# Kernel optimization log

Hardware: AMD Instinct MI355X
Metric: run time of the kernel (lower is better)

## Reference

```python
import jax, jax.numpy as jnp
import numpy as np

NUM_HEADS = 8
SPARSITY = 0.25
BOUNDARY_W = 0.5
LN_EPS = 1e-5


def setup_inputs() -> dict:
    key = jax.random.key(0)
    ks = jax.random.split(key, 16)
    B, C, H, W = 8, 256, 64, 64
    Ch = C // 4
    s = lambda *sh: 1.0 / np.sqrt(sh[-1])
    inp = {
        'x': jax.random.normal(ks[0], (B, C, H, W), jnp.float32),
        'boundary_map': jax.random.uniform(ks[1], (B, 1, H, W), jnp.float32),
        'imp_w1': jax.random.normal(ks[2], (Ch, C), jnp.float32) * s(C),
        'imp_b1': jnp.zeros((Ch,), jnp.float32),
        'imp_w2': jax.random.normal(ks[3], (1, Ch), jnp.float32) * s(Ch),
        'imp_b2': jnp.zeros((1,), jnp.float32),
        'wq': jax.random.normal(ks[4], (C, C), jnp.float32) * s(C),
        'bq': jnp.zeros((C,), jnp.float32),
        'wk': jax.random.normal(ks[5], (C, C), jnp.float32) * s(C),
        'bk': jnp.zeros((C,), jnp.float32),
        'wv': jax.random.normal(ks[6], (C, C), jnp.float32) * s(C),
        'bv': jnp.zeros((C,), jnp.float32),
        'wo': jax.random.normal(ks[7], (C, C), jnp.float32) * (0.1 * s(C)),
        'bo': jnp.zeros((C,), jnp.float32),
        'ln_g': jnp.ones((C,), jnp.float32),
        'ln_b': jnp.zeros((C,), jnp.float32),
    }
    return inp


def reference(x, boundary_map, imp_w1, imp_b1, imp_w2, imp_b2,
              wq, bq, wk, bk, wv, bv, wo, bo, ln_g, ln_b):
    B, C, H, W = x.shape
    N = H * W
    K = max(int(N * SPARSITY), 1)
    nh = NUM_HEADS
    hd = C // nh
    scale = hd ** -0.5

    # importance net: 1x1 conv -> GELU -> 1x1 conv -> sigmoid
    h = jnp.einsum('bchw,oc->bohw', x, imp_w1) + imp_b1[None, :, None, None]
    h = jax.nn.gelu(h, approximate=False)
    imp = jnp.einsum('bchw,oc->bohw', h, imp_w2) + imp_b2[None, :, None, None]
    importance = jax.nn.sigmoid(imp) + BOUNDARY_W * boundary_map  # [B,1,H,W]

    # top-K token selection
    _, top_idx = jax.lax.top_k(importance.reshape(B, N), K)  # [B,K]

    x_flat = x.transpose(0, 2, 3, 1).reshape(B, N, C)
    x_sp = jnp.take_along_axis(x_flat, top_idx[..., None], axis=1)  # [B,K,C]

    # sparse self-attention over K tokens
    q = (jnp.einsum('bkc,oc->bko', x_sp, wq) + bq).reshape(B, K, nh, hd)
    k = (jnp.einsum('bkc,oc->bko', x_sp, wk) + bk).reshape(B, K, nh, hd)
    v = (jnp.einsum('bkc,oc->bko', x_sp, wv) + bv).reshape(B, K, nh, hd)
    attn = jax.nn.softmax(jnp.einsum('bqhd,bkhd->bhqk', q, k) * scale, axis=-1)
    o = jnp.einsum('bhqk,bkhd->bqhd', attn, v).reshape(B, K, C)
    out_sp = jnp.einsum('bkc,oc->bko', o, wo) + bo

    # residual + LayerNorm
    y = out_sp + x_sp
    mu = jnp.mean(y, axis=-1, keepdims=True)
    var = jnp.mean(jnp.square(y - mu), axis=-1, keepdims=True)
    enh = (y - mu) * jax.lax.rsqrt(var + LN_EPS) * ln_g + ln_b  # [B,K,C]

    # scatter enhanced tokens back
    bidx = jnp.arange(B)[:, None]
    out_full = x_flat.at[bidx, top_idx].set(enh)
    out = out_full.reshape(B, H, W, C).transpose(0, 3, 1, 2)
    return out, importance
```

## Files before the change

kernel.cpp:

```cpp
#include <hip/hip_runtime.h>
#include <math.h>

#define B_ 8
#define C_ 256
#define N_ 4096
#define K_ 1024
#define NH_ 8
#define HD_ 32

typedef __attribute__((ext_vector_type(8))) short short8;
typedef __attribute__((ext_vector_type(8))) _Float16 half8;
typedef __attribute__((ext_vector_type(4))) _Float16 half4;
typedef __attribute__((ext_vector_type(4))) float f32x4;

#if __has_builtin(__builtin_amdgcn_exp2f)
#define EXPX(x) __builtin_amdgcn_exp2f(x)
#define QSCALE (0.17677669529663688f * 1.4426950408889634f)
#else
#define EXPX(x) __expf(x)
#define QSCALE 0.17677669529663688f
#endif

__device__ __forceinline__ unsigned bfr(float x){
  unsigned u = __float_as_uint(x);
  return (u + 0x7FFFu + ((u >> 16) & 1u)) >> 16;
}
__device__ __forceinline__ unsigned pk2(float lo, float hi){
  return bfr(lo) | (bfr(hi) << 16);
}
__device__ __forceinline__ unsigned hpk(float a, float b){
  _Float16 ha = (_Float16)a, hb = (_Float16)b;
  unsigned short ua = __builtin_bit_cast(unsigned short, ha);
  unsigned short ub = __builtin_bit_cast(unsigned short, hb);
  return (unsigned)ua | ((unsigned)ub << 16);
}
__device__ __forceinline__ half4 pk4rtz(float a, float b, float c, float d){
  auto lo = __builtin_amdgcn_cvt_pkrtz(a, b);
  auto hi = __builtin_amdgcn_cvt_pkrtz(c, d);
  uint2 u = make_uint2(__builtin_bit_cast(unsigned, lo), __builtin_bit_cast(unsigned, hi));
  return __builtin_bit_cast(half4, u);
}

__global__ __launch_bounds__(256) void w2h_kernel(
    const float* __restrict__ wq, const float* __restrict__ wk,
    const float* __restrict__ wv, const float* __restrict__ wo,
    unsigned short* __restrict__ wh)
{
  const float* src = blockIdx.y==0 ? wq : blockIdx.y==1 ? wk : blockIdx.y==2 ? wv : wo;
  const int e = (blockIdx.x*256 + threadIdx.x)*8;
  float4 a = *(const float4*)(src + e);
  float4 b = *(const float4*)(src + e + 4);
  uint4 o;
  o.x = hpk(a.x, a.y); o.y = hpk(a.z, a.w);
  o.z = hpk(b.x, b.y); o.w = hpk(b.z, b.w);
  *(uint4*)(wh + (size_t)blockIdx.y*65536 + e) = o;
}

__global__ __launch_bounds__(256) void imp_kernel(
    const float* __restrict__ x, const float* __restrict__ bmap,
    const float* __restrict__ w1, const float* __restrict__ b1,
    const float* __restrict__ w2, const float* __restrict__ b2,
    float* __restrict__ imp_out)
{
  __shared__ float xs[64][256];
  const int t = threadIdx.x;
  const int b = blockIdx.x >> 6, tile = blockIdx.x & 63;
  const int n0 = tile * 64;
  {
    const int i = t & 63, cg = t >> 6;
    const float* xb = x + (size_t)b*C_*N_ + n0 + i;
    const int ib = (i & 15) ^ (i >> 2);
    #pragma unroll 4
    for (int cc = 0; cc < 16; cc++){
      const int c0 = cg*64 + cc*4;
      float4 v;
      v.x = xb[(size_t)(c0+0)*N_];
      v.y = xb[(size_t)(c0+1)*N_];
      v.z = xb[(size_t)(c0+2)*N_];
      v.w = xb[(size_t)(c0+3)*N_];
      *(float4*)&xs[i][4*((cg*16+cc) ^ ib)] = v;
    }
  }
  __syncthreads();
  const int pg = t & 15, og = t >> 4;
  float acc[4][4];
  #pragma unroll
  for (int pp=0;pp<4;pp++)
    #pragma unroll
    for (int oo=0;oo<4;oo++) acc[pp][oo] = 0.f;
  int pb[4];
  #pragma unroll
  for (int pp=0;pp<4;pp++){ int p = 4*pg+pp; pb[pp] = (p&15)^(p>>2); }
  #pragma unroll 2
  for (int c8 = 0; c8 < 256; c8 += 8){
    const int G = c8 >> 2;
    float4 xa[4], xc[4];
    #pragma unroll
    for (int pp=0;pp<4;pp++){
      xa[pp] = *(const float4*)&xs[4*pg+pp][4*( G    ^ pb[pp])];
      xc[pp] = *(const float4*)&xs[4*pg+pp][4*((G+1) ^ pb[pp])];
    }
    float4 wa[4], wb[4];
    #pragma unroll
    for (int oo=0;oo<4;oo++){
      const float* wr = w1 + (size_t)(4*og+oo)*C_ + c8;
      wa[oo] = *(const float4*)wr;
      wb[oo] = *(const float4*)(wr+4);
    }
    #pragma unroll
    for (int pp=0;pp<4;pp++)
      #pragma unroll
      for (int oo=0;oo<4;oo++)
        acc[pp][oo] += xa[pp].x*wa[oo].x + xa[pp].y*wa[oo].y + xa[pp].z*wa[oo].z + xa[pp].w*wa[oo].w
                     + xc[pp].x*wb[oo].x + xc[pp].y*wb[oo].y + xc[pp].z*wb[oo].z + xc[pp].w*wb[oo].w;
  }
  float part[4] = {0.f,0.f,0.f,0.f};
  #pragma unroll
  for (int oo=0;oo<4;oo++){
    const int o = 4*og + oo;
    const float b1o = b1[o], w2o = w2[o];
    #pragma unroll
    for (int pp=0;pp<4;pp++){
      float a = acc[pp][oo] + b1o;
      float g = 0.5f*a*(1.f + erff(a*0.70710678118654752f));
      part[pp] += w2o*g;
    }
  }
  #pragma unroll
  for (int pp=0;pp<4;pp++){
    part[pp] += __shfl_xor(part[pp], 16);
    part[pp] += __shfl_xor(part[pp], 32);
  }
  __syncthreads();
  float* red = &xs[0][0];
  const int w = t >> 6;
  if ((t & 63) < 16){
    #pragma unroll
    for (int pp=0;pp<4;pp++) red[w*64 + 4*(t&15)+pp] = part[pp];
  }
  __syncthreads();
  if (t < 64){
    float s = red[t]+red[64+t]+red[128+t]+red[192+t] + b2[0];
    float sig = 1.f/(1.f+expf(-s));
    imp_out[(size_t)b*N_ + n0 + t] = sig + 0.5f*bmap[(size_t)b*N_ + n0 + t];
  }
}

__global__ __launch_bounds__(1024) void topk_kernel(const float* __restrict__ imp, int* __restrict__ tidx)
{
  __shared__ unsigned long long s[4096];
  __shared__ int idx[1024];
  const int b = blockIdx.x, t = threadIdx.x;
  const float* ib = imp + (size_t)b*N_;
  for (int m = t; m < N_; m += 1024){
    unsigned u = __float_as_uint(ib[m]);
    u = (u & 0x80000000u) ? ~u : (u | 0x80000000u);
    s[m] = ((unsigned long long)u << 32) | (unsigned)(~m);
  }
  for (int k = 2; k <= 4096; k <<= 1){
    for (int j = k >> 1; j > 0; j >>= 1){
      __syncthreads();
      #pragma unroll 2
      for (int m = t; m < 2048; m += 1024){
        int i = 2*m - (m & (j-1));
        int l = i + j;
        unsigned long long a = s[i], c = s[l];
        if ((a > c) == ((i & k) == 0)){ s[i] = c; s[l] = a; }
      }
    }
  }
  __syncthreads();
  idx[t] = (int)(~(unsigned)(s[3072 + t]));
  for (int k = 2; k <= 1024; k <<= 1){
    for (int j = k >> 1; j > 0; j >>= 1){
      __syncthreads();
      if (t < 512){
        int i = 2*t - (t & (j-1));
        int l = i + j;
        int a = idx[i], c = idx[l];
        if ((a > c) == ((i & k) == 0)){ idx[i] = c; idx[l] = a; }
      }
    }
  }
  __syncthreads();
  tidx[(size_t)b*K_ + t] = idx[t];
}

__global__ __launch_bounds__(512) void qkv_kernel(
    const float* __restrict__ x, const int* __restrict__ tidx,
    const unsigned short* __restrict__ wh,
    const float* __restrict__ bq, const float* __restrict__ bk, const float* __restrict__ bv,
    float* __restrict__ xsp, unsigned short* __restrict__ qbf,
    unsigned short* __restrict__ kbf, unsigned short* __restrict__ vtb)
{
  __shared__ unsigned short xsb[16][256];
  const int t = threadIdx.x;
  const int kt = blockIdx.x, b = blockIdx.y;
  const int tok0 = kt*16;
  {
    const int i = t & 15, jg = t >> 4;
    const int n = tidx[(size_t)b*K_ + tok0 + i];
    const float* xb = x + (size_t)b*C_*N_ + n;
    float v[8];
    #pragma unroll
    for (int u = 0; u < 8; u++) v[u] = xb[(size_t)(jg*8+u)*N_];
    float* xr = xsp + ((size_t)b*K_ + tok0 + i)*C_ + jg*8;
    *(float4*)(xr)     = make_float4(v[0],v[1],v[2],v[3]);
    *(float4*)(xr + 4) = make_float4(v[4],v[5],v[6],v[7]);
    uint4 pw;
    pw.x = hpk(v[0],v[1]); pw.y = hpk(v[2],v[3]);
    pw.z = hpk(v[4],v[5]); pw.w = hpk(v[6],v[7]);
    *(uint4*)((char*)&xsb[0][0] + i*512 + ((jg ^ (i&7))*16)) = pw;
  }
  __syncthreads();

  const int lane = t & 63, w = t >> 6;
  const int g = lane >> 4, c = lane & 15;

  f32x4 acc[3][2];
  #pragma unroll
  for (int s=0;s<3;s++)
    #pragma unroll
    for (int j=0;j<2;j++) acc[s][j] = (f32x4){0.f,0.f,0.f,0.f};

  #pragma unroll 1
  for (int ks = 0; ks < 8; ks++){
    half8 Xf = *(const half8*)((const char*)&xsb[0][0] + c*512 + (((4*ks+g) ^ (c&7))*16));
    half8 Wf[3][2];
    #pragma unroll
    for (int s=0;s<3;s++)
      #pragma unroll
      for (int j=0;j<2;j++)
        Wf[s][j] = *(const half8*)(wh + (size_t)s*65536 + (32*w + 16*j + c)*C_ + ks*32 + 8*g);
    acc[0][0] = __builtin_amdgcn_mfma_f32_16x16x32_f16(Wf[0][0], Xf, acc[0][0], 0,0,0);
    acc[0][1] = __builtin_amdgcn_mfma_f32_16x16x32_f16(Wf[0][1], Xf, acc[0][1], 0,0,0);
    acc[1][0] = __builtin_amdgcn_mfma_f32_16x16x32_f16(Wf[1][0], Xf, acc[1][0], 0,0,0);
    acc[1][1] = __builtin_amdgcn_mfma_f32_16x16x32_f16(Wf[1][1], Xf, acc[1][1], 0,0,0);
    acc[2][0] = __builtin_amdgcn_mfma_f32_16x16x32_f16(Xf, Wf[2][0], acc[2][0], 0,0,0);
    acc[2][1] = __builtin_amdgcn_mfma_f32_16x16x32_f16(Xf, Wf[2][1], acc[2][1], 0,0,0);
  }

  const int bh = b*NH_ + w;
  #pragma unroll
  for (int s=0;s<2;s++){
    const float* bias = s ? bk : bq;
    const float sc = s ? 1.f : QSCALE;
    unsigned short* dstb = s ? kbf : qbf;
    #pragma unroll
    for (int j=0;j<2;j++){
      f32x4 a = acc[s][j];
      float4 bb = *(const float4*)(bias + w*32 + 16*j + 4*g);
      unsigned lo = pk2((a[0]+bb.x)*sc, (a[1]+bb.y)*sc);
      unsigned hi = pk2((a[2]+bb.z)*sc, (a[3]+bb.w)*sc);
      unsigned short* dst = dstb + ((size_t)bh*K_ + tok0 + c)*HD_ + 16*j + 4*g;
      *(uint2*)dst = make_uint2(lo, hi);
    }
  }
  const int base32 = tok0 & ~31;
  const int half   = (tok0 >> 4) & 1;
  #pragma unroll
  for (int j=0;j<2;j++){
    f32x4 a = acc[2][j];
    const float bvv = bv[w*32 + 16*j + c];
    unsigned lo = hpk(a[0]+bvv, a[1]+bvv);
    unsigned hi = hpk(a[2]+bvv, a[3]+bvv);
    unsigned short* dst = vtb + ((size_t)bh*HD_ + 16*j + c)*K_ + base32 + 8*g + 4*half;
    *(uint2*)dst = make_uint2(lo, hi);
  }
}

__global__ __launch_bounds__(512) void attn_kernel(
    const unsigned short* __restrict__ qbf, const unsigned short* __restrict__ kbf,
    const unsigned short* __restrict__ vtb, unsigned short* __restrict__ ob)
{
  __shared__ float po[4][64][19];
  const int tid = threadIdx.x;
  const int t = tid & 63, w = tid >> 6;
  const int sp = w >> 2, qq = w & 3;
  const int flat = blockIdx.x;
  const int h = flat & 7;
  const int rest = flat >> 3;
  const int qt = rest & 7;
  const int b = rest >> 3;
  const int g = t >> 4, c = t & 15;
  const int bh = b*NH_ + h;
  const int q0 = qt*128 + qq*32;

  short8 Qf0 = *(const short8*)(qbf + ((size_t)bh*K_ + q0 + c)*HD_ + g*8);
  short8 Qf1 = *(const short8*)(qbf + ((size_t)bh*K_ + q0 + 16 + c)*HD_ + g*8);

  const int kbeg = sp*512;
  const unsigned short* kp  = kbf + (size_t)bh*K_*HD_ + (size_t)(kbeg + c)*HD_ + g*8;
  const unsigned short* vp0 = vtb + ((size_t)bh*HD_ + c)*K_ + kbeg + g*8;
  const unsigned short* vp1 = vp0 + (size_t)16*K_;

  const half4 ONES = {(_Float16)1.f, (_Float16)1.f, (_Float16)1.f, (_Float16)1.f};
  f32x4 ot00 = {0.f,0.f,0.f,0.f}, ot01 = {0.f,0.f,0.f,0.f};
  f32x4 ot10 = {0.f,0.f,0.f,0.f}, ot11 = {0.f,0.f,0.f,0.f};
  f32x4 otL0 = {0.f,0.f,0.f,0.f}, otL1 = {0.f,0.f,0.f,0.f};

  short8 K0c = *(const short8*)(kp);
  short8 K1c = *(const short8*)(kp + 16*HD_);
  half8  V0c = *(const half8*)(vp0);
  half8  V1c = *(const half8*)(vp1);

  #pragma unroll 2
  for (int it = 0; it < 16; ++it){
    kp += 32*HD_; vp0 += 32; vp1 += 32;
    short8 K0n = *(const short8*)(kp);
    short8 K1n = *(const short8*)(kp + 16*HD_);
    half8  V0n = *(const half8*)(vp0);
    half8  V1n = *(const half8*)(vp1);

    f32x4 z = {0.f,0.f,0.f,0.f};
    __builtin_amdgcn_s_setprio(1);
    f32x4 s00 = __builtin_amdgcn_mfma_f32_16x16x32_bf16(K0c, Qf0, z, 0, 0, 0);
    f32x4 s01 = __builtin_amdgcn_mfma_f32_16x16x32_bf16(K1c, Qf0, z, 0, 0, 0);
    f32x4 s10 = __builtin_amdgcn_mfma_f32_16x16x32_bf16(K0c, Qf1, z, 0, 0, 0);
    f32x4 s11 = __builtin_amdgcn_mfma_f32_16x16x32_bf16(K1c, Qf1, z, 0, 0, 0);
    __builtin_amdgcn_s_setprio(0);

    float p00[4], p01[4], p10[4], p11[4];
    #pragma unroll
    for (int r=0;r<4;r++){
      p00[r] = EXPX(s00[r]); p01[r] = EXPX(s01[r]);
      p10[r] = EXPX(s10[r]); p11[r] = EXPX(s11[r]);
    }

    half4 P00 = pk4rtz(p00[0], p00[1], p00[2], p00[3]);
    half4 P01 = pk4rtz(p01[0], p01[1], p01[2], p01[3]);
    half4 P10 = pk4rtz(p10[0], p10[1], p10[2], p10[3]);
    half4 P11 = pk4rtz(p11[0], p11[1], p11[2], p11[3]);

    half4 A0lo = __builtin_shufflevector(V0c, V0c, 0, 1, 2, 3);
    half4 A0hi = __builtin_shufflevector(V0c, V0c, 4, 5, 6, 7);
    half4 A1lo = __builtin_shufflevector(V1c, V1c, 0, 1, 2, 3);
    half4 A1hi = __builtin_shufflevector(V1c, V1c, 4, 5, 6, 7);

    __builtin_amdgcn_s_setprio(1);
    ot00 = __builtin_amdgcn_mfma_f32_16x16x16f16(A0lo, P00, ot00, 0, 0, 0);
    ot00 = __builtin_amdgcn_mfma_f32_16x16x16f16(A0hi, P01, ot00, 0, 0, 0);
    ot01 = __builtin_amdgcn_mfma_f32_16x16x16f16(A1lo, P00, ot01, 0, 0, 0);
    ot01 = __builtin_amdgcn_mfma_f32_16x16x16f16(A1hi, P01, ot01, 0, 0, 0);
    ot10 = __builtin_amdgcn_mfma_f32_16x16x16f16(A0lo, P10, ot10, 0, 0, 0);
    ot10 = __builtin_amdgcn_mfma_f32_16x16x16f16(A0hi, P11, ot10, 0, 0, 0);
    ot11 = __builtin_amdgcn_mfma_f32_16x16x16f16(A1lo, P10, ot11, 0, 0, 0);
    ot11 = __builtin_amdgcn_mfma_f32_16x16x16f16(A1hi, P11, ot11, 0, 0, 0);
    otL0 = __builtin_amdgcn_mfma_f32_16x16x16f16(ONES, P00, otL0, 0, 0, 0);
    otL0 = __builtin_amdgcn_mfma_f32_16x16x16f16(ONES, P01, otL0, 0, 0, 0);
    otL1 = __builtin_amdgcn_mfma_f32_16x16x16f16(ONES, P10, otL1, 0, 0, 0);
    otL1 = __builtin_amdgcn_mfma_f32_16x16x16f16(ONES, P11, otL1, 0, 0, 0);
    __builtin_amdgcn_s_setprio(0);

    K0c = K0n; K1c = K1n; V0c = V0n; V1c = V1n;
  }

  if (sp == 1){
    float* d = po[qq][t];
    d[0]=ot00[0]; d[1]=ot00[1]; d[2]=ot00[2];  d[3]=ot00[3];
    d[4]=ot01[0]; d[5]=ot01[1]; d[6]=ot01[2];  d[7]=ot01[3];
    d[8]=ot10[0]; d[9]=ot10[1]; d[10]=ot10[2]; d[11]=ot10[3];
    d[12]=ot11[0];d[13]=ot11[1];d[14]=ot11[2]; d[15]=ot11[3];
    d[16]=otL0[0]; d[17]=otL1[0];
  }
  __syncthreads();
  if (sp == 0){
    const float* d = po[qq][t];
    ot00[0]+=d[0]; ot00[1]+=d[1]; ot00[2]+=d[2];  ot00[3]+=d[3];
    ot01[0]+=d[4]; ot01[1]+=d[5]; ot01[2]+=d[6];  ot01[3]+=d[7];
    ot10[0]+=d[8]; ot10[1]+=d[9]; ot10[2]+=d[10]; ot10[3]+=d[11];
    ot11[0]+=d[12];ot11[1]+=d[13];ot11[2]+=d[14]; ot11[3]+=d[15];
    const float L0 = otL0[0] + d[16];
    const float L1 = otL1[0] + d[17];
    const float i0 = 1.f / L0, i1 = 1.f / L1;
    unsigned short* o0 = ob + ((size_t)b*K_ + q0 + c)*C_ + h*HD_;
    unsigned short* o1 = ob + ((size_t)b*K_ + q0 + 16 + c)*C_ + h*HD_;
    *(uint2*)(o0 + 4*g)      = make_uint2(hpk(ot00[0]*i0, ot00[1]*i0), hpk(ot00[2]*i0, ot00[3]*i0));
    *(uint2*)(o0 + 16 + 4*g) = make_uint2(hpk(ot01[0]*i0, ot01[1]*i0), hpk(ot01[2]*i0, ot01[3]*i0));
    *(uint2*)(o1 + 4*g)      = make_uint2(hpk(ot10[0]*i1, ot10[1]*i1), hpk(ot10[2]*i1, ot10[3]*i1));
    *(uint2*)(o1 + 16 + 4*g) = make_uint2(hpk(ot11[0]*i1, ot11[1]*i1), hpk(ot11[2]*i1, ot11[3]*i1));
  }
}

__global__ __launch_bounds__(512) void out_kernel(
    const unsigned short* __restrict__ ob, const float* __restrict__ xsp,
    const int* __restrict__ tidx, const unsigned short* __restrict__ woh, const float* __restrict__ bo,
    const float* __restrict__ lng, const float* __restrict__ lnb,
    float* __restrict__ out)
{
  __shared__ float red1[8][64], red2[8][64];
  __shared__ float mus[64], rss[64];
  __shared__ int nn[64];
  const int t = threadIdx.x;
  const int kt = blockIdx.x, b = blockIdx.y;
  const int tok0 = kt*64;
  const int lane = t & 63, w = t >> 6;
  const int g = lane >> 4, c = lane & 15;

  if (t < 64) nn[t] = tidx[(size_t)b*K_ + tok0 + t];

  f32x4 acc[2][4];
  #pragma unroll
  for (int j=0;j<2;j++)
    #pragma unroll
    for (int tt=0;tt<4;tt++) acc[j][tt] = (f32x4){0.f,0.f,0.f,0.f};

  const unsigned short* ob0 = ob + ((size_t)b*K_ + tok0)*C_;
  const unsigned short* wr0 = woh + (32*w + c)*C_;

  #pragma unroll 1
  for (int ks = 0; ks < 8; ks++){
    half8 Wf0 = *(const half8*)(wr0 + ks*32 + 8*g);
    half8 Wf1 = *(const half8*)(wr0 + 16*C_ + ks*32 + 8*g);
    #pragma unroll
    for (int tt=0;tt<4;tt++){
      half8 Of = *(const half8*)(ob0 + (size_t)(16*tt + c)*C_ + ks*32 + 8*g);
      acc[0][tt] = __builtin_amdgcn_mfma_f32_16x16x32_f16(Wf0, Of, acc[0][tt], 0,0,0);
      acc[1][tt] = __builtin_amdgcn_mfma_f32_16x16x32_f16(Wf1, Of, acc[1][tt], 0,0,0);
    }
  }

  float4 bb[2];
  #pragma unroll
  for (int j=0;j<2;j++) bb[j] = *(const float4*)(bo + 32*w + 16*j + 4*g);
  #pragma unroll
  for (int tt=0;tt<4;tt++){
    const float* xr = xsp + ((size_t)b*K_ + tok0 + 16*tt + c)*C_ + 32*w + 4*g;
    #pragma unroll
    for (int j=0;j<2;j++){
      float4 xv = *(const float4*)(xr + 16*j);
      acc[j][tt][0] += bb[j].x + xv.x;
      acc[j][tt][1] += bb[j].y + xv.y;
      acc[j][tt][2] += bb[j].z + xv.z;
      acc[j][tt][3] += bb[j].w + xv.w;
    }
  }

  #pragma unroll
  for (int tt=0;tt<4;tt++){
    float s1 = 0.f, s2 = 0.f;
    #pragma unroll
    for (int j=0;j<2;j++)
      #pragma unroll
      for (int r=0;r<4;r++){ float y = acc[j][tt][r]; s1 += y; s2 += y*y; }
    s1 += __shfl_xor(s1, 16); s2 += __shfl_xor(s2, 16);
    s1 += __shfl_xor(s1, 32); s2 += __shfl_xor(s2, 32);
    if (g == 0){ red1[w][16*tt + c] = s1; red2[w][16*tt + c] = s2; }
  }
  __syncthreads();
  if (t < 64){
    float a = 0.f, q2 = 0.f;
    #pragma unroll
    for (int ww=0;ww<8;ww++){ a += red1[ww][t]; q2 += red2[ww][t]; }
    float mu = a*(1.f/256.f);
    float var = q2*(1.f/256.f) - mu*mu;
    mus[t] = mu;
    rss[t] = rsqrtf(var + 1e-5f);
  }
  __syncthreads();

  float4 gv[2], bv2[2];
  #pragma unroll
  for (int j=0;j<2;j++){
    gv[j]  = *(const float4*)(lng + 32*w + 16*j + 4*g);
    bv2[j] = *(const float4*)(lnb + 32*w + 16*j + 4*g);
  }
  float* outb = out + (size_t)b*C_*N_;
  #pragma unroll
  for (int tt=0;tt<4;tt++){
    const int tok = 16*tt + c;
    const float mu = mus[tok], rs = rss[tok];
    const int n = nn[tok];
    #pragma unroll
    for (int j=0;j<2;j++){
      const int oc0 = 32*w + 16*j + 4*g;
      const float* gvp = (const float*)&gv[j];
      const float* bvp = (const float*)&bv2[j];
      #pragma unroll
      for (int r=0;r<4;r++)
        outb[(size_t)(oc0 + r)*N_ + n] = (acc[j][tt][r]-mu)*rs*gvp[r] + bvp[r];
    }
  }
}

extern "C" void kernel_launch(void* const* d_in, const int* in_sizes, int n_in,
                              void* d_out, int out_size, void* d_ws, size_t ws_size,
                              hipStream_t stream)
{
  const float* x    = (const float*)d_in[0];
  const float* bmap = (const float*)d_in[1];
  const float* w1   = (const float*)d_in[2];
  const float* b1   = (const float*)d_in[3];
  const float* w2   = (const float*)d_in[4];
  const float* b2   = (const float*)d_in[5];
  const float* wq   = (const float*)d_in[6];
  const float* bq   = (const float*)d_in[7];
  const float* wk   = (const float*)d_in[8];
  const float* bk   = (const float*)d_in[9];
  const float* wv   = (const float*)d_in[10];
  const float* bv   = (const float*)d_in[11];
  const float* wo   = (const float*)d_in[12];
  const float* bo   = (const float*)d_in[13];
  const float* lng  = (const float*)d_in[14];
  const float* lnb  = (const float*)d_in[15];

  float* out = (float*)d_out;
  float* imp_out = out + (size_t)B_*C_*N_;

  char* wsb = (char*)d_ws;
  int*   tidx = (int*)wsb;
  float* xsp  = (float*)(wsb + 65536);
  unsigned short* ob16 = (unsigned short*)(xsp + (size_t)B_*K_*C_);
  unsigned short* qbf = ob16 + 2*(size_t)B_*K_*C_;
  unsigned short* kbf = qbf + (size_t)B_*NH_*K_*HD_;
  unsigned short* vtb = kbf + (size_t)B_*NH_*K_*HD_;
  unsigned short* wh  = vtb + (size_t)B_*NH_*K_*HD_;

  hipMemcpyAsync(out, x, (size_t)B_*C_*N_*sizeof(float), hipMemcpyDeviceToDevice, stream);
  w2h_kernel <<<dim3(32, 4),    dim3(256),  0, stream>>>(wq, wk, wv, wo, wh);
  imp_kernel <<<dim3(512),      dim3(256),  0, stream>>>(x, bmap, w1, b1, w2, b2, imp_out);
  topk_kernel<<<dim3(8),        dim3(1024), 0, stream>>>(imp_out, tidx);
  qkv_kernel <<<dim3(64, 8),    dim3(512),  0, stream>>>(x, tidx, wh, bq, bk, bv, xsp, qbf, kbf, vtb);
  attn_kernel<<<dim3(512),      dim3(512),  0, stream>>>(qbf, kbf, vtb, ob16);
  out_kernel <<<dim3(16, 8),    dim3(512),  0, stream>>>(ob16, xsp, tidx, wh + 3*65536, bo, lng, lnb, out);
}
```

Before: 159.6 us.

## Fuse residual copy into importance kernel and replace top-k index sort with compaction

The separate device-to-device copy of x into the output is folded into the importance kernel, which now writes x to the output while staging it, and runs with 512 threads. The second bitonic sort over selected indices in top-k becomes a threshold test plus prefix-sum compaction, which keeps indices in ascending order without another sort. The attention loop is unrolled by hand with two-stage register prefetch, and the output kernel processes 32 tokens per block so more blocks are launched. Together these target extra memory traffic, sort synchronisation and latency hiding, at the cost of more register pressure and threshold logic that depends on unique keys.

```diff
diff --git a/kernel.cpp b/kernel.cpp
--- a/kernel.cpp
+++ b/kernel.cpp
@@ -56,11 +56,11 @@
   *(uint4*)(wh + (size_t)blockIdx.y*65536 + e) = o;
 }
 
-__global__ __launch_bounds__(256) void imp_kernel(
+__global__ __launch_bounds__(512) void imp_kernel(
     const float* __restrict__ x, const float* __restrict__ bmap,
     const float* __restrict__ w1, const float* __restrict__ b1,
     const float* __restrict__ w2, const float* __restrict__ b2,
-    float* __restrict__ imp_out)
+    float* __restrict__ imp_out, float* __restrict__ outx)
 {
   __shared__ float xs[64][256];
   const int t = threadIdx.x;
@@ -69,25 +69,30 @@
   {
     const int i = t & 63, cg = t >> 6;
     const float* xb = x + (size_t)b*C_*N_ + n0 + i;
-    const int ib = (i & 15) ^ (i >> 2);
-    #pragma unroll 4
-    for (int cc = 0; cc < 16; cc++){
-      const int c0 = cg*64 + cc*4;
+    float* ox = outx + (size_t)b*C_*N_ + n0 + i;
+    const int ib2 = (i & 15) ^ (i >> 2);
+    #pragma unroll
+    for (int cc = 0; cc < 8; cc++){
+      const int c0 = cg*32 + cc*4;
       float4 v;
       v.x = xb[(size_t)(c0+0)*N_];
       v.y = xb[(size_t)(c0+1)*N_];
       v.z = xb[(size_t)(c0+2)*N_];
       v.w = xb[(size_t)(c0+3)*N_];
-      *(float4*)&xs[i][4*((cg*16+cc) ^ ib)] = v;
-    }
-  }
-  __syncthreads();
-  const int pg = t & 15, og = t >> 4;
-  float acc[4][4];
+      *(float4*)&xs[i][4*((cg*8+cc) ^ ib2)] = v;
+      ox[(size_t)(c0+0)*N_] = v.x;
+      ox[(size_t)(c0+1)*N_] = v.y;
+      ox[(size_t)(c0+2)*N_] = v.z;
+      ox[(size_t)(c0+3)*N_] = v.w;
+    }
+  }
+  __syncthreads();
+  const int pg = t & 15, og2 = t >> 4;
+  float acc[4][2];
   #pragma unroll
   for (int pp=0;pp<4;pp++)
     #pragma unroll
-    for (int oo=0;oo<4;oo++) acc[pp][oo] = 0.f;
+    for (int oo=0;oo<2;oo++) acc[pp][oo] = 0.f;
   int pb[4];
   #pragma unroll
   for (int pp=0;pp<4;pp++){ int p = 4*pg+pp; pb[pp] = (p&15)^(p>>2); }
@@ -100,24 +105,24 @@
       xa[pp] = *(const float4*)&xs[4*pg+pp][4*( G    ^ pb[pp])];
       xc[pp] = *(const float4*)&xs[4*pg+pp][4*((G+1) ^ pb[pp])];
     }
-    float4 wa[4], wb[4];
-    #pragma unroll
-    for (int oo=0;oo<4;oo++){
-      const float* wr = w1 + (size_t)(4*og+oo)*C_ + c8;
+    float4 wa[2], wb[2];
+    #pragma unroll
+    for (int oo=0;oo<2;oo++){
+      const float* wr = w1 + (size_t)(2*og2+oo)*C_ + c8;
       wa[oo] = *(const float4*)wr;
       wb[oo] = *(const float4*)(wr+4);
     }
     #pragma unroll
     for (int pp=0;pp<4;pp++)
       #pragma unroll
-      for (int oo=0;oo<4;oo++)
+      for (int oo=0;oo<2;oo++)
         acc[pp][oo] += xa[pp].x*wa[oo].x + xa[pp].y*wa[oo].y + xa[pp].z*wa[oo].z + xa[pp].w*wa[oo].w
                      + xc[pp].x*wb[oo].x + xc[pp].y*wb[oo].y + xc[pp].z*wb[oo].z + xc[pp].w*wb[oo].w;
   }
   float part[4] = {0.f,0.f,0.f,0.f};
   #pragma unroll
-  for (int oo=0;oo<4;oo++){
-    const int o = 4*og + oo;
+  for (int oo=0;oo<2;oo++){
+    const int o = 2*og2 + oo;
     const float b1o = b1[o], w2o = w2[o];
     #pragma unroll
     for (int pp=0;pp<4;pp++){
@@ -133,14 +138,17 @@
   }
   __syncthreads();
   float* red = &xs[0][0];
-  const int w = t >> 6;
-  if ((t & 63) < 16){
-    #pragma unroll
-    for (int pp=0;pp<4;pp++) red[w*64 + 4*(t&15)+pp] = part[pp];
+  const int w = t >> 6, lane = t & 63;
+  if (lane < 16){
+    #pragma unroll
+    for (int pp=0;pp<4;pp++) red[w*64 + 4*lane + pp] = part[pp];
   }
   __syncthreads();
   if (t < 64){
-    float s = red[t]+red[64+t]+red[128+t]+red[192+t] + b2[0];
+    float s = 0.f;
+    #pragma unroll
+    for (int ww=0;ww<8;ww++) s += red[ww*64 + t];
+    s += b2[0];
     float sig = 1.f/(1.f+expf(-s));
     imp_out[(size_t)b*N_ + n0 + t] = sig + 0.5f*bmap[(size_t)b*N_ + n0 + t];
   }
@@ -149,7 +157,7 @@
 __global__ __launch_bounds__(1024) void topk_kernel(const float* __restrict__ imp, int* __restrict__ tidx)
 {
   __shared__ unsigned long long s[4096];
-  __shared__ int idx[1024];
+  __shared__ int ws2[16];
   const int b = blockIdx.x, t = threadIdx.x;
   const float* ib = imp + (size_t)b*N_;
   for (int m = t; m < N_; m += 1024){
@@ -170,20 +178,34 @@
     }
   }
   __syncthreads();
-  idx[t] = (int)(~(unsigned)(s[3072 + t]));
-  for (int k = 2; k <= 1024; k <<= 1){
-    for (int j = k >> 1; j > 0; j >>= 1){
-      __syncthreads();
-      if (t < 512){
-        int i = 2*t - (t & (j-1));
-        int l = i + j;
-        int a = idx[i], c = idx[l];
-        if ((a > c) == ((i & k) == 0)){ idx[i] = c; idx[l] = a; }
-      }
-    }
-  }
-  __syncthreads();
-  tidx[(size_t)b*K_ + t] = idx[t];
+  const unsigned long long thr = s[3072];
+  int sel[4]; int cnt = 0;
+  #pragma unroll
+  for (int u2 = 0; u2 < 4; u2++){
+    const int m = 4*t + u2;
+    unsigned u = __float_as_uint(ib[m]);
+    u = (u & 0x80000000u) ? ~u : (u | 0x80000000u);
+    unsigned long long key = ((unsigned long long)u << 32) | (unsigned)(~m);
+    sel[u2] = (key >= thr) ? 1 : 0;
+    cnt += sel[u2];
+  }
+  int incl = cnt;
+  #pragma unroll
+  for (int d2 = 1; d2 < 64; d2 <<= 1){
+    int v2 = __shfl_up(incl, d2);
+    if ((t & 63) >= d2) incl += v2;
+  }
+  if ((t & 63) == 63) ws2[t >> 6] = incl;
+  __syncthreads();
+  int base = 0;
+  const int wv2 = t >> 6;
+  #pragma unroll
+  for (int ww = 0; ww < 16; ww++) if (ww < wv2) base += ws2[ww];
+  int pos = base + incl - cnt;
+  #pragma unroll
+  for (int u2 = 0; u2 < 4; u2++){
+    if (sel[u2]) tidx[(size_t)b*K_ + pos++] = 4*t + u2;
+  }
 }
 
 __global__ __launch_bounds__(512) void qkv_kernel(
@@ -299,61 +321,71 @@
   f32x4 ot10 = {0.f,0.f,0.f,0.f}, ot11 = {0.f,0.f,0.f,0.f};
   f32x4 otL0 = {0.f,0.f,0.f,0.f}, otL1 = {0.f,0.f,0.f,0.f};
 
-  short8 K0c = *(const short8*)(kp);
-  short8 K1c = *(const short8*)(kp + 16*HD_);
-  half8  V0c = *(const half8*)(vp0);
-  half8  V1c = *(const half8*)(vp1);
-
-  #pragma unroll 2
-  for (int it = 0; it < 16; ++it){
+#define ATTN_STEP(K0c,K1c,V0c,V1c) do {                                           \
+    f32x4 z = {0.f,0.f,0.f,0.f};                                                  \
+    __builtin_amdgcn_s_setprio(1);                                                \
+    f32x4 s00 = __builtin_amdgcn_mfma_f32_16x16x32_bf16(K0c, Qf0, z, 0, 0, 0);    \
+    f32x4 s01 = __builtin_amdgcn_mfma_f32_16x16x32_bf16(K1c, Qf0, z, 0, 0, 0);    \
+    f32x4 s10 = __builtin_amdgcn_mfma_f32_16x16x32_bf16(K0c, Qf1, z, 0, 0, 0);    \
+    f32x4 s11 = __builtin_amdgcn_mfma_f32_16x16x32_bf16(K1c, Qf1, z, 0, 0, 0);    \
+    __builtin_amdgcn_s_setprio(0);                                                \
+    float p00[4], p01[4], p10[4], p11[4];                                         \
+    _Pragma("unroll")                                                             \
+    for (int r=0;r<4;r++){                                                        \
+      p00[r] = EXPX(s00[r]); p01[r] = EXPX(s01[r]);                               \
+      p10[r] = EXPX(s10[r]); p11[r] = EXPX(s11[r]);                               \
+    }                                                                             \
+    half4 P00 = pk4rtz(p00[0], p00[1], p00[2], p00[3]);                           \
+    half4 P01 = pk4rtz(p01[0], p01[1], p01[2], p01[3]);                           \
+    half4 P10 = pk4rtz(p10[0], p10[1], p10[2], p10[3]);                           \
+    half4 P11 = pk4rtz(p11[0], p11[1], p11[2], p11[3]);                           \
+    half4 A0lo = __builtin_shufflevector(V0c, V0c, 0, 1, 2, 3);                   \
+    half4 A0hi = __builtin_shufflevector(V0c, V0c, 4, 5, 6, 7);                   \
+    half4 A1lo = __builtin_shufflevector(V1c, V1c, 0, 1, 2, 3);                   \
+    half4 A1hi = __builtin_shufflevector(V1c, V1c, 4, 5, 6, 7);                   \
+    __builtin_amdgcn_s_setprio(1);                                                \
+    ot00 = __builtin_amdgcn_mfma_f32_16x16x16f16(A0lo, P00, ot00, 0, 0, 0);       \
+    ot00 = __builtin_amdgcn_mfma_f32_16x16x16f16(A0hi, P01, ot00, 0, 0, 0);       \
+    ot01 = __builtin_amdgcn_mfma_f32_16x16x16f16(A1lo, P00, ot01, 0, 0, 0);       \
+    ot01 = __builtin_amdgcn_mfma_f32_16x16x16f16(A1hi, P01, ot01, 0, 0, 0);       \
+    ot10 = __builtin_amdgcn_mfma_f32_16x16x16f16(A0lo, P10, ot10, 0, 0, 0);       \
+    ot10 = __builtin_amdgcn_mfma_f32_16x16x16f16(A0hi, P11, ot10, 0, 0, 0);       \
+    ot11 = __builtin_amdgcn_mfma_f32_16x16x16f16(A1lo, P10, ot11, 0, 0, 0);       \
+    ot11 = __builtin_amdgcn_mfma_f32_16x16x16f16(A1hi, P11, ot11, 0, 0, 0);       \
+    otL0 = __builtin_amdgcn_mfma_f32_16x16x16f16(ONES, P00, otL0, 0, 0, 0);       \
+    otL0 = __builtin_amdgcn_mfma_f32_16x16x16f16(ONES, P01, otL0, 0, 0, 0);       \
+    otL1 = __builtin_amdgcn_mfma_f32_16x16x16f16(ONES, P10, otL1, 0, 0, 0);       \
+    otL1 = __builtin_amdgcn_mfma_f32_16x16x16f16(ONES, P11, otL1, 0, 0, 0);       \
+    __builtin_amdgcn_s_setprio(0);                                                \
+  } while(0)
+
+  short8 K0a = *(const short8*)(kp);
+  short8 K1a = *(const short8*)(kp + 16*HD_);
+  half8  V0a = *(const half8*)(vp0);
+  half8  V1a = *(const half8*)(vp1);
+  kp += 32*HD_; vp0 += 32; vp1 += 32;
+  short8 K0b = *(const short8*)(kp);
+  short8 K1b = *(const short8*)(kp + 16*HD_);
+  half8  V0b = *(const half8*)(vp0);
+  half8  V1b = *(const half8*)(vp1);
+
+  for (int it = 0; it < 16; it += 2){
     kp += 32*HD_; vp0 += 32; vp1 += 32;
     short8 K0n = *(const short8*)(kp);
     short8 K1n = *(const short8*)(kp + 16*HD_);
     half8  V0n = *(const half8*)(vp0);
     half8  V1n = *(const half8*)(vp1);
-
-    f32x4 z = {0.f,0.f,0.f,0.f};
-    __builtin_amdgcn_s_setprio(1);
-    f32x4 s00 = __builtin_amdgcn_mfma_f32_16x16x32_bf16(K0c, Qf0, z, 0, 0, 0);
-    f32x4 s01 = __builtin_amdgcn_mfma_f32_16x16x32_bf16(K1c, Qf0, z, 0, 0, 0);
-    f32x4 s10 = __builtin_amdgcn_mfma_f32_16x16x32_bf16(K0c, Qf1, z, 0, 0, 0);
-    f32x4 s11 = __builtin_amdgcn_mfma_f32_16x16x32_bf16(K1c, Qf1, z, 0, 0, 0);
-    __builtin_amdgcn_s_setprio(0);
-
-    float p00[4], p01[4], p10[4], p11[4];
-    #pragma unroll
-    for (int r=0;r<4;r++){
-      p00[r] = EXPX(s00[r]); p01[r] = EXPX(s01[r]);
-      p10[r] = EXPX(s10[r]); p11[r] = EXPX(s11[r]);
-    }
-
-    half4 P00 = pk4rtz(p00[0], p00[1], p00[2], p00[3]);
-    half4 P01 = pk4rtz(p01[0], p01[1], p01[2], p01[3]);
-    half4 P10 = pk4rtz(p10[0], p10[1], p10[2], p10[3]);
-    half4 P11 = pk4rtz(p11[0], p11[1], p11[2], p11[3]);
-
-    half4 A0lo = __builtin_shufflevector(V0c, V0c, 0, 1, 2, 3);
-    half4 A0hi = __builtin_shufflevector(V0c, V0c, 4, 5, 6, 7);
-    half4 A1lo = __builtin_shufflevector(V1c, V1c, 0, 1, 2, 3);
-    half4 A1hi = __builtin_shufflevector(V1c, V1c, 4, 5, 6, 7);
-
-    __builtin_amdgcn_s_setprio(1);
-    ot00 = __builtin_amdgcn_mfma_f32_16x16x16f16(A0lo, P00, ot00, 0, 0, 0);
-    ot00 = __builtin_amdgcn_mfma_f32_16x16x16f16(A0hi, P01, ot00, 0, 0, 0);
-    ot01 = __builtin_amdgcn_mfma_f32_16x16x16f16(A1lo, P00, ot01, 0, 0, 0);
-    ot01 = __builtin_amdgcn_mfma_f32_16x16x16f16(A1hi, P01, ot01, 0, 0, 0);
-    ot10 = __builtin_amdgcn_mfma_f32_16x16x16f16(A0lo, P10, ot10, 0, 0, 0);
-    ot10 = __builtin_amdgcn_mfma_f32_16x16x16f16(A0hi, P11, ot10, 0, 0, 0);
-    ot11 = __builtin_amdgcn_mfma_f32_16x16x16f16(A1lo, P10, ot11, 0, 0, 0);
-    ot11 = __builtin_amdgcn_mfma_f32_16x16x16f16(A1hi, P11, ot11, 0, 0, 0);
-    otL0 = __builtin_amdgcn_mfma_f32_16x16x16f16(ONES, P00, otL0, 0, 0, 0);
-    otL0 = __builtin_amdgcn_mfma_f32_16x16x16f16(ONES, P01, otL0, 0, 0, 0);
-    otL1 = __builtin_amdgcn_mfma_f32_16x16x16f16(ONES, P10, otL1, 0, 0, 0);
-    otL1 = __builtin_amdgcn_mfma_f32_16x16x16f16(ONES, P11, otL1, 0, 0, 0);
-    __builtin_amdgcn_s_setprio(0);
-
-    K0c = K0n; K1c = K1n; V0c = V0n; V1c = V1n;
-  }
+    ATTN_STEP(K0a, K1a, V0a, V1a);
+    K0a = K0n; K1a = K1n; V0a = V0n; V1a = V1n;
+    kp += 32*HD_; vp0 += 32; vp1 += 32;
+    short8 K0m = *(const short8*)(kp);
+    short8 K1m = *(const short8*)(kp + 16*HD_);
+    half8  V0m = *(const half8*)(vp0);
+    half8  V1m = *(const half8*)(vp1);
+    ATTN_STEP(K0b, K1b, V0b, V1b);
+    K0b = K0m; K1b = K1m; V0b = V0m; V1b = V1m;
+  }
+#undef ATTN_STEP
 
   if (sp == 1){
     float* d = po[qq][t];
@@ -388,22 +420,22 @@
     const float* __restrict__ lng, const float* __restrict__ lnb,
     float* __restrict__ out)
 {
-  __shared__ float red1[8][64], red2[8][64];
-  __shared__ float mus[64], rss[64];
-  __shared__ int nn[64];
+  __shared__ float red1[8][32], red2[8][32];
+  __shared__ float mus[32], rss[32];
+  __shared__ int nn[32];
   const int t = threadIdx.x;
   const int kt = blockIdx.x, b = blockIdx.y;
-  const int tok0 = kt*64;
+  const int tok0 = kt*32;
   const int lane = t & 63, w = t >> 6;
   const int g = lane >> 4, c = lane & 15;
 
-  if (t < 64) nn[t] = tidx[(size_t)b*K_ + tok0 + t];
-
-  f32x4 acc[2][4];
+  if (t < 32) nn[t] = tidx[(size_t)b*K_ + tok0 + t];
+
+  f32x4 acc[2][2];
   #pragma unroll
   for (int j=0;j<2;j++)
     #pragma unroll
-    for (int tt=0;tt<4;tt++) acc[j][tt] = (f32x4){0.f,0.f,0.f,0.f};
+    for (int tt=0;tt<2;tt++) acc[j][tt] = (f32x4){0.f,0.f,0.f,0.f};
 
   const unsigned short* ob0 = ob + ((size_t)b*K_ + tok0)*C_;
   const unsigned short* wr0 = woh + (32*w + c)*C_;
@@ -413,7 +445,7 @@
     half8 Wf0 = *(const half8*)(wr0 + ks*32 + 8*g);
     half8 Wf1 = *(const half8*)(wr0 + 16*C_ + ks*32 + 8*g);
     #pragma unroll
-    for (int tt=0;tt<4;tt++){
+    for (int tt=0;tt<2;tt++){
       half8 Of = *(const half8*)(ob0 + (size_t)(16*tt + c)*C_ + ks*32 + 8*g);
       acc[0][tt] = __builtin_amdgcn_mfma_f32_16x16x32_f16(Wf0, Of, acc[0][tt], 0,0,0);
       acc[1][tt] = __builtin_amdgcn_mfma_f32_16x16x32_f16(Wf1, Of, acc[1][tt], 0,0,0);
@@ -424,7 +456,7 @@
   #pragma unroll
   for (int j=0;j<2;j++) bb[j] = *(const float4*)(bo + 32*w + 16*j + 4*g);
   #pragma unroll
-  for (int tt=0;tt<4;tt++){
+  for (int tt=0;tt<2;tt++){
     const float* xr = xsp + ((size_t)b*K_ + tok0 + 16*tt + c)*C_ + 32*w + 4*g;
     #pragma unroll
     for (int j=0;j<2;j++){
@@ -437,7 +469,7 @@
   }
 
   #pragma unroll
-  for (int tt=0;tt<4;tt++){
+  for (int tt=0;tt<2;tt++){
     float s1 = 0.f, s2 = 0.f;
     #pragma unroll
     for (int j=0;j<2;j++)
@@ -448,7 +480,7 @@
     if (g == 0){ red1[w][16*tt + c] = s1; red2[w][16*tt + c] = s2; }
   }
   __syncthreads();
-  if (t < 64){
+  if (t < 32){
     float a = 0.f, q2 = 0.f;
     #pragma unroll
     for (int ww=0;ww<8;ww++){ a += red1[ww][t]; q2 += red2[ww][t]; }
@@ -467,7 +499,7 @@
   }
   float* outb = out + (size_t)b*C_*N_;
   #pragma unroll
-  for (int tt=0;tt<4;tt++){
+  for (int tt=0;tt<2;tt++){
     const int tok = 16*tt + c;
     const float mu = mus[tok], rs = rss[tok];
     const int n = nn[tok];
@@ -516,11 +548,10 @@
   unsigned short* vtb = kbf + (size_t)B_*NH_*K_*HD_;
   unsigned short* wh  = vtb + (size_t)B_*NH_*K_*HD_;
 
-  hipMemcpyAsync(out, x, (size_t)B_*C_*N_*sizeof(float), hipMemcpyDeviceToDevice, stream);
   w2h_kernel <<<dim3(32, 4),    dim3(256),  0, stream>>>(wq, wk, wv, wo, wh);
-  imp_kernel <<<dim3(512),      dim3(256),  0, stream>>>(x, bmap, w1, b1, w2, b2, imp_out);
+  imp_kernel <<<dim3(512),      dim3(512),  0, stream>>>(x, bmap, w1, b1, w2, b2, imp_out, out);
   topk_kernel<<<dim3(8),        dim3(1024), 0, stream>>>(imp_out, tidx);
   qkv_kernel <<<dim3(64, 8),    dim3(512),  0, stream>>>(x, tidx, wh, bq, bk, bv, xsp, qbf, kbf, vtb);
   attn_kernel<<<dim3(512),      dim3(512),  0, stream>>>(qbf, kbf, vtb, ob16);
-  out_kernel <<<dim3(16, 8),    dim3(512),  0, stream>>>(ob16, xsp, tidx, wh + 3*65536, bo, lng, lnb, out);
-}
+  out_kernel <<<dim3(32, 8),    dim3(512),  0, stream>>>(ob16, xsp, tidx, wh + 3*65536, bo, lng, lnb, out);
+}
```

Measured after the change: 147.9 us. 7.3% less time.
